# Kernel optimization log

Measured on AMD Instinct MI355X. Metric: run time of the kernel, lower is better.

Reference implementation:

```python
import jax, jax.numpy as jnp
import numpy as np

B, T, D, H = 8, 1024, 512, 8
HD = D // H  # per-head hidden = embed_dim // n_head = 64
EPS = 1e-5


def setup_inputs() -> dict:
    key = jax.random.key(0)
    ks = jax.random.split(key, 8)
    x = jax.random.normal(ks[0], (B, T, D), dtype=jnp.float32)
    sc = 1.0 / np.sqrt(D)
    Wq = jax.random.normal(ks[1], (D, H * HD), dtype=jnp.float32) * sc
    Wk = jax.random.normal(ks[2], (D, H * HD), dtype=jnp.float32) * sc
    Wp = jax.random.normal(ks[3], (H * HD, D), dtype=jnp.float32) * sc
    bq = jnp.zeros((H * HD,), jnp.float32)
    bk = jnp.zeros((H * HD,), jnp.float32)
    bp = jnp.zeros((D,), jnp.float32)
    w_mlp = jax.random.normal(ks[4], (2 * HD,), dtype=jnp.float32) * 0.1
    ln_g = jnp.ones((D,), jnp.float32)
    ln_b = jnp.zeros((D,), jnp.float32)
    return {"x": x, "Wq": Wq, "bq": bq, "Wk": Wk, "bk": bk,
            "Wp": Wp, "bp": bp, "w_mlp": w_mlp, "ln_g": ln_g, "ln_b": ln_b}


def reference(x, Wq, bq, Wk, bk, Wp, bp, w_mlp, ln_g, ln_b):
    b, t, d = x.shape
    h, hd = H, HD
    # q/k projections, split into heads: [B,T,H,hd]
    qx = (x @ Wq + bq).reshape(b, t, h, hd)
    kx = (x @ Wk + bk).reshape(b, t, h, hd)
    # MLP score: tanh(concat(k_j, q_i) . w) == tanh(k_j.w[:hd] + q_i.w[hd:])
    k_s = jnp.einsum('bkhd,d->bkh', kx, w_mlp[:hd])   # [B,K,H]
    q_s = jnp.einsum('bqhd,d->bqh', qx, w_mlp[hd:])   # [B,Q,H]
    score = jnp.tanh(q_s[:, :, None, :] + k_s[:, None, :, :])  # [B,Q,K,H]
    attn = jax.nn.softmax(score, axis=2)  # softmax over k_len
    # values are the key projection kx (bmm(score, kx) in original)
    out = jnp.einsum('bqkh,bkhd->bqhd', attn, kx).reshape(b, t, h * hd)
    out = out @ Wp + bp  # output projection (dropout is identity at eval)
    # residual + LayerNorm
    y = x + out
    mu = jnp.mean(y, axis=-1, keepdims=True)
    var = jnp.var(y, axis=-1, keepdims=True)
    yn = (y - mu) * jax.lax.rsqrt(var + EPS)
    return yn * ln_g + ln_b
```

## Files before the change

kernel.cpp:

```cpp
#include <hip/hip_runtime.h>
#include <cstddef>

#define TT 1024
#define DDIM 512
#define HH 8
#define NND 128
#define NS 68

typedef __attribute__((ext_vector_type(8))) short bfrag;
typedef __attribute__((ext_vector_type(4))) float facc;

#define SC2   2.8853900817779268f
#define L2E   1.4426950408889634f

static __device__ __forceinline__ unsigned bfrne(float f) {
    unsigned u = __float_as_uint(f);
    return (u + 0x7fffu + ((u >> 16) & 1u)) >> 16;
}
static __device__ __forceinline__ unsigned pack2rne(float a, float b) {
    return bfrne(a) | (bfrne(b) << 16);
}
static __device__ __forceinline__ unsigned pack2hu(float a, float b) {
    return ((__float_as_uint(a) + 0x8000u) >> 16) |
           ((__float_as_uint(b) + 0x8000u) & 0xffff0000u);
}
static __device__ __forceinline__ void gl2lds16(const void* g, void* l) {
    __builtin_amdgcn_global_load_lds(
        (const __attribute__((address_space(1))) unsigned int*)g,
        (__attribute__((address_space(3))) unsigned int*)l, 16, 0, 0);
}
static __device__ __forceinline__ float wfun(float z2) {
    float t = __builtin_amdgcn_exp2f(z2);
    float r = __builtin_amdgcn_rcpf(t + 1.f);
    return __builtin_amdgcn_exp2f(fmaf(r, -2.f * L2E, L2E));
}

__global__ __launch_bounds__(256) void prepare_kernel(
    const float* __restrict__ x, const float* __restrict__ Wk,
    const float* __restrict__ Wp, const float* __restrict__ Wq,
    const float* __restrict__ bq, const float* __restrict__ wm,
    unsigned short* __restrict__ xb, unsigned short* __restrict__ WkT,
    unsigned short* __restrict__ WpT, unsigned short* __restrict__ vq2b,
    float* __restrict__ qsb2)
{
    const int bx = blockIdx.x, tid = threadIdx.x;
    if (bx < 2048) {
        const int lane = tid & 63, wave = tid >> 6;
        const int row = bx * 4 + wave;
        const float4* xr = (const float4*)(x + (size_t)row * DDIM);
        float4 x0 = xr[lane * 2], x1 = xr[lane * 2 + 1];
        uint4 st;
        st.x = pack2rne(x0.x, x0.y); st.y = pack2rne(x0.z, x0.w);
        st.z = pack2rne(x1.x, x1.y); st.w = pack2rne(x1.z, x1.w);
        int p = lane ^ (row & 7);
        *(uint4*)(xb + (size_t)row * DDIM + p * 8) = st;
    } else if (bx < 2176) {
        int idx = bx - 2048;
        const float* src = (idx & 64) ? Wp : Wk;
        unsigned short* dst = (idx & 64) ? WpT : WkT;
        idx &= 63;
        const int n0 = (idx & 7) * 64, k0 = (idx >> 3) * 64;
        __shared__ float sT[64][65];
        #pragma unroll
        for (int it = 0; it < 4; ++it) {
            int task = it * 256 + tid;
            int kr = task >> 4, c4 = (task & 15) * 4;
            float4 v = *(const float4*)(src + (size_t)(k0 + kr) * DDIM + n0 + c4);
            sT[kr][c4] = v.x; sT[kr][c4 + 1] = v.y; sT[kr][c4 + 2] = v.z; sT[kr][c4 + 3] = v.w;
        }
        __syncthreads();
        #pragma unroll
        for (int it = 0; it < 2; ++it) {
            int task = it * 256 + tid;
            int n = task >> 3, kg = task & 7;
            unsigned u[4];
            #pragma unroll
            for (int jj = 0; jj < 4; ++jj)
                u[jj] = pack2rne(sT[kg * 8 + jj * 2][n], sT[kg * 8 + jj * 2 + 1][n]);
            int p = ((k0 >> 3) + kg) ^ (n & 7);
            uint4 st; st.x = u[0]; st.y = u[1]; st.z = u[2]; st.w = u[3];
            *(uint4*)(dst + (size_t)(n0 + n) * DDIM + p * 8) = st;
        }
    } else {
        int idx = (bx - 2176) * 256 + tid;
        int h = idx >> 9, d = idx & 511;
        float s = 0.f;
        #pragma unroll 8
        for (int j = 0; j < 64; ++j)
            s = fmaf(Wq[(size_t)d * DDIM + h * 64 + j], wm[64 + j], s);
        vq2b[h * DDIM + d] = (unsigned short)bfrne(s * SC2);
        if (idx < HH) {
            float sb = 0.f;
            for (int j = 0; j < 64; ++j)
                sb = fmaf(bq[idx * 64 + j], wm[64 + j], sb);
            qsb2[idx] = sb * SC2;
        }
    }
}

__global__ __launch_bounds__(256) void gemm1_kernel(
    const unsigned short* __restrict__ A, const unsigned short* __restrict__ B,
    const float* __restrict__ bias, unsigned short* __restrict__ kxTg,
    float* __restrict__ ks2, const float* __restrict__ wm,
    const unsigned short* __restrict__ vq2b, const float* __restrict__ qsb2,
    float* __restrict__ qs2)
{
    __shared__ __align__(16) unsigned short smem[17408];
    unsigned short* sA = smem;
    unsigned short* sB = smem + 8192;
    const int tid = threadIdx.x, lane = tid & 63, wave = tid >> 6;
    const int l15 = lane & 15, quad = lane >> 4;
    const int wr = wave >> 1, wc = wave & 1;
    const int row0 = blockIdx.x * 128, colpair = blockIdx.y;
    const int h = colpair * 2 + wc, n0 = colpair * 128;

    facc acc[4][4]; facc accq[4];
    #pragma unroll
    for (int i = 0; i < 4; ++i) {
        #pragma unroll
        for (int j = 0; j < 4; ++j) { acc[i][j][0]=0.f; acc[i][j][1]=0.f; acc[i][j][2]=0.f; acc[i][j][3]=0.f; }
        accq[i][0]=0.f; accq[i][1]=0.f; accq[i][2]=0.f; accq[i][3]=0.f;
    }

    for (int k0 = 0; k0 < 512; k0 += 64) {
        #pragma unroll
        for (int it = 0; it < 4; ++it) {
            int g = it * 256 + tid;
            int r = g >> 3, kg = g & 7;
            gl2lds16(A + (size_t)(row0 + r) * 512 + k0 + kg * 8, &sA[g * 8]);
            gl2lds16(B + (size_t)(n0 + r) * 512 + k0 + kg * 8, &sB[g * 8]);
        }
        __syncthreads();
        #pragma unroll
        for (int ks_ = 0; ks_ < 2; ++ks_) {
            int slot = (ks_ * 4 + quad) ^ (l15 & 7);
            bfrag a[4], b[4];
            #pragma unroll
            for (int i = 0; i < 4; ++i) {
                a[i] = *(const bfrag*)&sA[(wr * 64 + i * 16 + l15) * 64 + slot * 8];
                b[i] = *(const bfrag*)&sB[(wc * 64 + i * 16 + l15) * 64 + slot * 8];
            }
            bfrag bvq = *(const bfrag*)(vq2b + h * 512 + k0 + ks_ * 32 + quad * 8);
            #pragma unroll
            for (int i = 0; i < 4; ++i) {
                #pragma unroll
                for (int nt = 0; nt < 4; ++nt)
                    acc[i][nt] = __builtin_amdgcn_mfma_f32_16x16x32_bf16(a[i], b[nt], acc[i][nt], 0, 0, 0);
                accq[i] = __builtin_amdgcn_mfma_f32_16x16x32_bf16(a[i], bvq, accq[i], 0, 0, 0);
            }
        }
        __syncthreads();
    }

    const int bb = row0 >> 10, t0 = row0 & 1023;
    const float qsbh = qsb2[h];
    float bvv[4], wmv[4];
    #pragma unroll
    for (int nt = 0; nt < 4; ++nt) {
        bvv[nt] = bias[h * 64 + nt * 16 + l15];
        wmv[nt] = wm[nt * 16 + l15] * SC2;
    }
    float part[4][4];
    #pragma unroll
    for (int i = 0; i < 4; ++i)
        #pragma unroll
        for (int r = 0; r < 4; ++r) part[i][r] = 0.f;

    unsigned short* eT = smem + wc * 8704;
    #pragma unroll
    for (int i = 0; i < 4; ++i) {
        int tr = wr * 64 + i * 16 + quad * 4;
        #pragma unroll
        for (int nt = 0; nt < 4; ++nt) {
            int d = nt * 16 + l15;
            float v0 = acc[i][nt][0] + bvv[nt], v1 = acc[i][nt][1] + bvv[nt];
            float v2 = acc[i][nt][2] + bvv[nt], v3 = acc[i][nt][3] + bvv[nt];
            part[i][0] = fmaf(wmv[nt], v0, part[i][0]);
            part[i][1] = fmaf(wmv[nt], v1, part[i][1]);
            part[i][2] = fmaf(wmv[nt], v2, part[i][2]);
            part[i][3] = fmaf(wmv[nt], v3, part[i][3]);
            *(unsigned*)&eT[d * 136 + tr]     = pack2rne(v0, v1);
            *(unsigned*)&eT[d * 136 + tr + 2] = pack2rne(v2, v3);
        }
    }
    #pragma unroll
    for (int i = 0; i < 4; ++i)
        #pragma unroll
        for (int r = 0; r < 4; ++r) {
            float p = part[i][r];
            p += __shfl_xor(p, 1); p += __shfl_xor(p, 2);
            p += __shfl_xor(p, 4); p += __shfl_xor(p, 8);
            if (l15 == 0) {
                size_t o = (size_t)(bb * HH + h) * TT + t0 + wr * 64 + i * 16 + quad * 4 + r;
                ks2[o] = p;
                qs2[o] = accq[i][r] + qsbh;
            }
        }
    __syncthreads();
    #pragma unroll
    for (int it = 0; it < 8; ++it) {
        int task = it * 256 + tid;
        int hh = task >> 10, rem = task & 1023;
        int col = rem >> 4, seg = rem & 15;
        uint4 v = *(const uint4*)&smem[hh * 8704 + col * 136 + seg * 8];
        int hg = colpair * 2 + hh;
        int g = (t0 >> 3) + seg;
        int p = g ^ (col & 7);
        *(uint4*)(kxTg + ((size_t)(bb * HH + hg) * 64 + col) * TT + p * 8) = v;
    }
}

__global__ __launch_bounds__(256) void attn_kernel(
    const unsigned short* __restrict__ kxTg, const float* __restrict__ qs2,
    const float* __restrict__ ks2, unsigned short* __restrict__ attb)
{
    __shared__ __align__(16) unsigned short kxT[64 * 256];
    __shared__ float ksc[1024];
    __shared__ float redl[8];
    __shared__ __align__(16) float nodes[NND * NS];
    const int bh = blockIdx.x, thalf = blockIdx.y;
    const int b = bh >> 3, h = bh & 7;
    const int tid = threadIdx.x, lane = tid & 63, wave = tid >> 6;
    const int l15 = lane & 15, quad = lane >> 4;

    ((float4*)ksc)[tid] = ((const float4*)(ks2 + (size_t)bh * TT))[tid];
    float4 q4 = ((const float4*)(qs2 + (size_t)bh * TT))[tid];
    float mn = fminf(fminf(q4.x, q4.y), fminf(q4.z, q4.w));
    float mx = fmaxf(fmaxf(q4.x, q4.y), fmaxf(q4.z, q4.w));
    #pragma unroll
    for (int off = 32; off > 0; off >>= 1) {
        mn = fminf(mn, __shfl_xor(mn, off));
        mx = fmaxf(mx, __shfl_xor(mx, off));
    }
    if (lane == 0) { redl[wave] = mn; redl[4 + wave] = mx; }
    __syncthreads();
    const float mnv = fminf(fminf(redl[0], redl[1]), fminf(redl[2], redl[3]));
    const float mxv = fmaxf(fmaxf(redl[4], redl[5]), fmaxf(redl[6], redl[7]));
    const float h2v = (mxv - mnv) * (1.f / 127.f);
    const float inv127v = 127.f / fmaxf(mxv - mnv, 1e-12f);
    const float zA = mnv + (wave * 16 + l15) * h2v;
    const float zB = zA + 64.f * h2v;

    const unsigned short* kxbase = kxTg + (size_t)bh * 64 * TT;
    facc acc[2][4]; facc accZ[2];
    #pragma unroll
    for (int g = 0; g < 2; ++g) {
        #pragma unroll
        for (int i = 0; i < 4; ++i) { acc[g][i][0]=0.f; acc[g][i][1]=0.f; acc[g][i][2]=0.f; acc[g][i][3]=0.f; }
        accZ[g][0]=0.f; accZ[g][1]=0.f; accZ[g][2]=0.f; accZ[g][3]=0.f;
    }
    bfrag ones;
    #pragma unroll
    for (int j = 0; j < 8; ++j) ones[j] = (short)0x3F80;

    for (int ck = 0; ck < 4; ++ck) {
        #pragma unroll
        for (int it = 0; it < 8; ++it) {
            int g = it * 256 + tid;
            int d = g >> 5, j = g & 31;
            gl2lds16(kxbase + (size_t)d * TT + ck * 256 + j * 8, &kxT[g * 8]);
        }
        __syncthreads();
        #pragma unroll
        for (int kst = 0; kst < 8; ++kst) {
            const float* kvp = &ksc[ck * 256 + kst * 32 + quad * 8];
            float4 kv0 = *(const float4*)kvp;
            float4 kv1 = *(const float4*)(kvp + 4);
            int slot = (kst * 4 + quad) ^ (l15 & 7);
            bfrag bf_[4];
            #pragma unroll
            for (int dt = 0; dt < 4; ++dt)
                bf_[dt] = *(const bfrag*)&kxT[(dt * 16 + l15) * 256 + slot * 8];
            #pragma unroll
            for (int g = 0; g < 2; ++g) {
                float z = g ? zB : zA;
                union { unsigned u[4]; bfrag f; } afu;
                afu.u[0] = pack2hu(wfun(z + kv0.x), wfun(z + kv0.y));
                afu.u[1] = pack2hu(wfun(z + kv0.z), wfun(z + kv0.w));
                afu.u[2] = pack2hu(wfun(z + kv1.x), wfun(z + kv1.y));
                afu.u[3] = pack2hu(wfun(z + kv1.z), wfun(z + kv1.w));
                #pragma unroll
                for (int dt = 0; dt < 4; ++dt)
                    acc[g][dt] = __builtin_amdgcn_mfma_f32_16x16x32_bf16(afu.f, bf_[dt], acc[g][dt], 0, 0, 0);
                accZ[g] = __builtin_amdgcn_mfma_f32_16x16x32_bf16(afu.f, ones, accZ[g], 0, 0, 0);
            }
        }
        __syncthreads();
    }
    #pragma unroll
    for (int g = 0; g < 2; ++g) {
        #pragma unroll
        for (int r = 0; r < 4; ++r) {
            int node = g * 64 + wave * 16 + quad * 4 + r;
            #pragma unroll
            for (int dt = 0; dt < 4; ++dt)
                nodes[node * NS + dt * 16 + l15] = acc[g][dt][r];
            if (l15 == 0) nodes[node * NS + 64] = accZ[g][r];
        }
    }
    __syncthreads();

    const float* qsp = qs2 + (size_t)bh * TT;
    #pragma unroll 2
    for (int it = 0; it < 32; ++it) {
        int task = it * 256 + tid;
        int t = thalf * 512 + (task >> 4), dp = task & 15;
        float qv = qsp[t];
        float u = (qv - mnv) * inv127v;
        int i = (int)floorf(u) - 1;
        i = i < 0 ? 0 : (i > NND - 4 ? NND - 4 : i);
        float s = u - (float)i;
        float s1 = s - 1.f, s2 = s - 2.f, s3 = s - 3.f;
        float w0 = -s1 * s2 * s3 * (1.f / 6.f);
        float w1 = s * s2 * s3 * 0.5f;
        float w2 = -s * s1 * s3 * 0.5f;
        float w3 = s * s1 * s2 * (1.f / 6.f);
        const float* base = &nodes[i * NS];
        float4 v0 = *(const float4*)(base + 4 * dp);
        float4 v1 = *(const float4*)(base + NS + 4 * dp);
        float4 v2 = *(const float4*)(base + 2 * NS + 4 * dp);
        float4 v3 = *(const float4*)(base + 3 * NS + 4 * dp);
        float zz = w0 * base[64] + w1 * base[NS + 64] + w2 * base[2 * NS + 64] + w3 * base[3 * NS + 64];
        float ox = w0 * v0.x + w1 * v1.x + w2 * v2.x + w3 * v3.x;
        float oy = w0 * v0.y + w1 * v1.y + w2 * v2.y + w3 * v3.y;
        float oz = w0 * v0.z + w1 * v1.z + w2 * v2.z + w3 * v3.z;
        float ow = w0 * v0.w + w1 * v1.w + w2 * v2.w + w3 * v3.w;
        float rz = __builtin_amdgcn_rcpf(zz);
        uint2 st;
        st.x = pack2rne(ox * rz, oy * rz);
        st.y = pack2rne(oz * rz, ow * rz);
        int row = b * TT + t;
        int col = h * 64 + 4 * dp;
        int p = (col >> 3) ^ (row & 7);
        *(uint2*)&attb[(size_t)row * DDIM + p * 8 + (col & 7)] = st;
    }
}

__global__ __launch_bounds__(256) void gemm2_kernel(
    const unsigned short* __restrict__ A, const unsigned short* __restrict__ B,
    const float* __restrict__ bias, unsigned short* __restrict__ yb)
{
    __shared__ __align__(16) unsigned short smem[17408];
    unsigned short* sA = smem;
    unsigned short* sB = smem + 8192;
    const int tid = threadIdx.x, lane = tid & 63, wave = tid >> 6;
    const int l15 = lane & 15, quad = lane >> 4;
    const int wr = wave >> 1, wc = wave & 1;
    const int row0 = blockIdx.x * 128, col0 = blockIdx.y * 128;

    facc acc[4][4];
    #pragma unroll
    for (int i = 0; i < 4; ++i)
        #pragma unroll
        for (int j = 0; j < 4; ++j) { acc[i][j][0]=0.f; acc[i][j][1]=0.f; acc[i][j][2]=0.f; acc[i][j][3]=0.f; }

    for (int k0 = 0; k0 < 512; k0 += 64) {
        #pragma unroll
        for (int it = 0; it < 4; ++it) {
            int g = it * 256 + tid;
            int r = g >> 3, kg = g & 7;
            gl2lds16(A + (size_t)(row0 + r) * 512 + k0 + kg * 8, &sA[g * 8]);
            gl2lds16(B + (size_t)(col0 + r) * 512 + k0 + kg * 8, &sB[g * 8]);
        }
        __syncthreads();
        #pragma unroll
        for (int ks_ = 0; ks_ < 2; ++ks_) {
            int slot = (ks_ * 4 + quad) ^ (l15 & 7);
            bfrag a[4], b[4];
            #pragma unroll
            for (int i = 0; i < 4; ++i) {
                a[i] = *(const bfrag*)&sA[(wr * 64 + i * 16 + l15) * 64 + slot * 8];
                b[i] = *(const bfrag*)&sB[(wc * 64 + i * 16 + l15) * 64 + slot * 8];
            }
            #pragma unroll
            for (int i = 0; i < 4; ++i)
                #pragma unroll
                for (int nt = 0; nt < 4; ++nt)
                    acc[i][nt] = __builtin_amdgcn_mfma_f32_16x16x32_bf16(a[i], b[nt], acc[i][nt], 0, 0, 0);
        }
        __syncthreads();
    }
    float bvv[4];
    #pragma unroll
    for (int nt = 0; nt < 4; ++nt) bvv[nt] = bias[col0 + wc * 64 + nt * 16 + l15];
    unsigned short* yT = smem;
    #pragma unroll
    for (int i = 0; i < 4; ++i) {
        #pragma unroll
        for (int nt = 0; nt < 4; ++nt) {
            int col = wc * 64 + nt * 16 + l15;
            #pragma unroll
            for (int r = 0; r < 4; ++r) {
                int row = wr * 64 + i * 16 + quad * 4 + r;
                yT[row * 136 + col] = (unsigned short)bfrne(acc[i][nt][r] + bvv[nt]);
            }
        }
    }
    __syncthreads();
    #pragma unroll
    for (int it = 0; it < 8; ++it) {
        int task = it * 256 + tid;
        int row = task >> 4, seg = task & 15;
        uint4 v = *(const uint4*)&yT[row * 136 + seg * 8];
        *(uint4*)(yb + (size_t)(row0 + row) * DDIM + col0 + seg * 8) = v;
    }
}

__global__ __launch_bounds__(256) void ln_kernel(
    const unsigned short* __restrict__ yb, const unsigned short* __restrict__ xb,
    const float* __restrict__ g, const float* __restrict__ bet,
    float* __restrict__ out)
{
    const int tid = threadIdx.x, lane = tid & 63, wave = tid >> 6;
    const int row = blockIdx.x * 4 + wave;
    uint4 pv = *(const uint4*)(yb + (size_t)row * DDIM + lane * 8);
    int pgr = lane ^ (row & 7);
    uint4 xv = *(const uint4*)(xb + (size_t)row * DDIM + pgr * 8);
    float y[8];
    const unsigned* pu = (const unsigned*)&pv;
    const unsigned* xu = (const unsigned*)&xv;
    #pragma unroll
    for (int j = 0; j < 4; ++j) {
        y[2*j]   = __uint_as_float(pu[j] << 16)        + __uint_as_float(xu[j] << 16);
        y[2*j+1] = __uint_as_float(pu[j] & 0xffff0000u) + __uint_as_float(xu[j] & 0xffff0000u);
    }
    float s = 0.f, s2 = 0.f;
    #pragma unroll
    for (int i = 0; i < 8; ++i) { s += y[i]; s2 = fmaf(y[i], y[i], s2); }
    #pragma unroll
    for (int off = 32; off > 0; off >>= 1) {
        s += __shfl_xor(s, off);
        s2 += __shfl_xor(s2, off);
    }
    float mu = s * (1.f / 512.f);
    float var = s2 * (1.f / 512.f) - mu * mu;
    float inv = rsqrtf(var + 1e-5f);
    const float4* gp = (const float4*)(g + lane * 8);
    const float4* bp = (const float4*)(bet + lane * 8);
    float4 g0 = gp[0], g1 = gp[1], b0 = bp[0], b1 = bp[1];
    float4 o0, o1;
    o0.x = (y[0] - mu) * inv * g0.x + b0.x; o0.y = (y[1] - mu) * inv * g0.y + b0.y;
    o0.z = (y[2] - mu) * inv * g0.z + b0.z; o0.w = (y[3] - mu) * inv * g0.w + b0.w;
    o1.x = (y[4] - mu) * inv * g1.x + b1.x; o1.y = (y[5] - mu) * inv * g1.y + b1.y;
    o1.z = (y[6] - mu) * inv * g1.z + b1.z; o1.w = (y[7] - mu) * inv * g1.w + b1.w;
    float4* op = (float4*)(out + (size_t)row * DDIM);
    op[lane * 2] = o0; op[lane * 2 + 1] = o1;
}

extern "C" void kernel_launch(void* const* d_in, const int* in_sizes, int n_in,
                              void* d_out, int out_size, void* d_ws, size_t ws_size,
                              hipStream_t stream)
{
    const float* x    = (const float*)d_in[0];
    const float* Wq   = (const float*)d_in[1];
    const float* bq   = (const float*)d_in[2];
    const float* Wk   = (const float*)d_in[3];
    const float* bk   = (const float*)d_in[4];
    const float* Wp   = (const float*)d_in[5];
    const float* bp   = (const float*)d_in[6];
    const float* wm   = (const float*)d_in[7];
    const float* ln_g = (const float*)d_in[8];
    const float* ln_b = (const float*)d_in[9];
    float* out = (float*)d_out;

    float* ws = (float*)d_ws;
    float*          qsb2 = ws;
    unsigned short* vq2b = (unsigned short*)(ws + 64);
    unsigned short* WkT  = (unsigned short*)(ws + 2112);
    unsigned short* WpT  = (unsigned short*)(ws + 133184);
    unsigned short* xb   = (unsigned short*)(ws + 264256);
    unsigned short* kxTg = (unsigned short*)(ws + 2361408);
    float*          qs2  = ws + 4458560;
    float*          ks2  = ws + 4524096;
    unsigned short* attb = (unsigned short*)(ws + 4589632);
    unsigned short* yb   = (unsigned short*)(ws + 6686784);

    prepare_kernel<<<2192, 256, 0, stream>>>(x, Wk, Wp, Wq, bq, wm,
                                             xb, WkT, WpT, vq2b, qsb2);
    gemm1_kernel<<<dim3(64, 4), 256, 0, stream>>>(xb, WkT, bk, kxTg, ks2, wm,
                                                  vq2b, qsb2, qs2);
    attn_kernel<<<dim3(64, 2), 256, 0, stream>>>(kxTg, qs2, ks2, attb);
    gemm2_kernel<<<dim3(64, 4), 256, 0, stream>>>(attb, WpT, bp, yb);
    ln_kernel<<<2048, 256, 0, stream>>>(yb, xb, ln_g, ln_b, out);
}
```

Measured before the change: 153.7 us.

## Double-buffer LDS tiles in both GEMMs and attention with async prefetch

Gives gemm1, gemm2 and attn_kernel double-buffered shared-memory tiles, so the next K-chunk is loaded with global-to-LDS copies while the current one is consumed. The old sync-load-sync loop becomes a manual vmcnt wait plus raw barriers. gemm1 also stages the vq2b vector in LDS instead of reading it from global memory on every step, and bias/wm loads are hoisted ahead of the main loop. The cost is roughly double the LDS per block, which may reduce occupancy, and more fragile hand-written waitcnt synchronisation.

```diff
diff --git a/kernel.cpp b/kernel.cpp
--- a/kernel.cpp
+++ b/kernel.cpp
@@ -105,15 +105,22 @@
     const unsigned short* __restrict__ vq2b, const float* __restrict__ qsb2,
     float* __restrict__ qs2)
 {
-    __shared__ __align__(16) unsigned short smem[17408];
-    unsigned short* sA = smem;
-    unsigned short* sB = smem + 8192;
+    __shared__ __align__(16) unsigned short smem[33792];
+    unsigned short* svq = smem + 32768;
     const int tid = threadIdx.x, lane = tid & 63, wave = tid >> 6;
     const int l15 = lane & 15, quad = lane >> 4;
     const int wr = wave >> 1, wc = wave & 1;
     const int row0 = blockIdx.x * 128, colpair = blockIdx.y;
     const int h = colpair * 2 + wc, n0 = colpair * 128;
 
+    const float qsbh = qsb2[h];
+    float bvv[4], wmv[4];
+    #pragma unroll
+    for (int nt = 0; nt < 4; ++nt) {
+        bvv[nt] = bias[h * 64 + nt * 16 + l15];
+        wmv[nt] = wm[nt * 16 + l15] * SC2;
+    }
+
     facc acc[4][4]; facc accq[4];
     #pragma unroll
     for (int i = 0; i < 4; ++i) {
@@ -122,15 +129,34 @@
         accq[i][0]=0.f; accq[i][1]=0.f; accq[i][2]=0.f; accq[i][3]=0.f;
     }
 
-    for (int k0 = 0; k0 < 512; k0 += 64) {
+    if (tid < 128)
+        gl2lds16(vq2b + colpair * 1024 + tid * 8, &svq[tid * 8]);
+
+    auto stage = [&](int sel, int k0) {
+        unsigned short* dA = smem + sel * 16384;
+        unsigned short* dB = dA + 8192;
         #pragma unroll
         for (int it = 0; it < 4; ++it) {
             int g = it * 256 + tid;
             int r = g >> 3, kg = g & 7;
-            gl2lds16(A + (size_t)(row0 + r) * 512 + k0 + kg * 8, &sA[g * 8]);
-            gl2lds16(B + (size_t)(n0 + r) * 512 + k0 + kg * 8, &sB[g * 8]);
-        }
-        __syncthreads();
+            gl2lds16(A + (size_t)(row0 + r) * 512 + k0 + kg * 8, &dA[g * 8]);
+            gl2lds16(B + (size_t)(n0 + r) * 512 + k0 + kg * 8, &dB[g * 8]);
+        }
+    };
+
+    stage(0, 0);
+    for (int kt = 0; kt < 8; ++kt) {
+        const int sel = kt & 1;
+        if (kt < 7) {
+            stage(sel ^ 1, (kt + 1) * 64);
+            asm volatile("s_waitcnt vmcnt(8)" ::: "memory");
+        } else {
+            asm volatile("s_waitcnt vmcnt(0)" ::: "memory");
+        }
+        __builtin_amdgcn_s_barrier();
+        __builtin_amdgcn_sched_barrier(0);
+        const unsigned short* sA = smem + sel * 16384;
+        const unsigned short* sB = sA + 8192;
         #pragma unroll
         for (int ks_ = 0; ks_ < 2; ++ks_) {
             int slot = (ks_ * 4 + quad) ^ (l15 & 7);
@@ -140,7 +166,7 @@
                 a[i] = *(const bfrag*)&sA[(wr * 64 + i * 16 + l15) * 64 + slot * 8];
                 b[i] = *(const bfrag*)&sB[(wc * 64 + i * 16 + l15) * 64 + slot * 8];
             }
-            bfrag bvq = *(const bfrag*)(vq2b + h * 512 + k0 + ks_ * 32 + quad * 8);
+            bfrag bvq = *(const bfrag*)&svq[wc * 512 + kt * 64 + ks_ * 32 + quad * 8];
             #pragma unroll
             for (int i = 0; i < 4; ++i) {
                 #pragma unroll
@@ -149,17 +175,12 @@
                 accq[i] = __builtin_amdgcn_mfma_f32_16x16x32_bf16(a[i], bvq, accq[i], 0, 0, 0);
             }
         }
-        __syncthreads();
-    }
+        __builtin_amdgcn_s_barrier();
+        __builtin_amdgcn_sched_barrier(0);
+    }
+    asm volatile("" ::: "memory");
 
     const int bb = row0 >> 10, t0 = row0 & 1023;
-    const float qsbh = qsb2[h];
-    float bvv[4], wmv[4];
-    #pragma unroll
-    for (int nt = 0; nt < 4; ++nt) {
-        bvv[nt] = bias[h * 64 + nt * 16 + l15];
-        wmv[nt] = wm[nt * 16 + l15] * SC2;
-    }
     float part[4][4];
     #pragma unroll
     for (int i = 0; i < 4; ++i)
@@ -214,7 +235,7 @@
     const unsigned short* __restrict__ kxTg, const float* __restrict__ qs2,
     const float* __restrict__ ks2, unsigned short* __restrict__ attb)
 {
-    __shared__ __align__(16) unsigned short kxT[64 * 256];
+    __shared__ __align__(16) unsigned short kxT[2 * 64 * 256];
     __shared__ float ksc[1024];
     __shared__ float redl[8];
     __shared__ __align__(16) float nodes[NND * NS];
@@ -222,9 +243,22 @@
     const int b = bh >> 3, h = bh & 7;
     const int tid = threadIdx.x, lane = tid & 63, wave = tid >> 6;
     const int l15 = lane & 15, quad = lane >> 4;
-
-    ((float4*)ksc)[tid] = ((const float4*)(ks2 + (size_t)bh * TT))[tid];
-    float4 q4 = ((const float4*)(qs2 + (size_t)bh * TT))[tid];
+    const unsigned short* kxbase = kxTg + (size_t)bh * 64 * TT;
+
+    auto stage = [&](int sel, int ck) {
+        unsigned short* dst = kxT + sel * 16384;
+        #pragma unroll
+        for (int it = 0; it < 8; ++it) {
+            int g = it * 256 + tid;
+            int d = g >> 5, j = g & 31;
+            gl2lds16(kxbase + (size_t)d * TT + ck * 256 + j * 8, &dst[g * 8]);
+        }
+    };
+
+    float4 ks4 = ((const float4*)(ks2 + (size_t)bh * TT))[tid];
+    float4 q4  = ((const float4*)(qs2 + (size_t)bh * TT))[tid];
+    stage(0, 0);
+    ((float4*)ksc)[tid] = ks4;
     float mn = fminf(fminf(q4.x, q4.y), fminf(q4.z, q4.w));
     float mx = fmaxf(fmaxf(q4.x, q4.y), fmaxf(q4.z, q4.w));
     #pragma unroll
@@ -233,7 +267,9 @@
         mx = fmaxf(mx, __shfl_xor(mx, off));
     }
     if (lane == 0) { redl[wave] = mn; redl[4 + wave] = mx; }
-    __syncthreads();
+    asm volatile("s_waitcnt lgkmcnt(0)" ::: "memory");
+    __builtin_amdgcn_s_barrier();
+    __builtin_amdgcn_sched_barrier(0);
     const float mnv = fminf(fminf(redl[0], redl[1]), fminf(redl[2], redl[3]));
     const float mxv = fmaxf(fmaxf(redl[4], redl[5]), fmaxf(redl[6], redl[7]));
     const float h2v = (mxv - mnv) * (1.f / 127.f);
@@ -241,7 +277,6 @@
     const float zA = mnv + (wave * 16 + l15) * h2v;
     const float zB = zA + 64.f * h2v;
 
-    const unsigned short* kxbase = kxTg + (size_t)bh * 64 * TT;
     facc acc[2][4]; facc accZ[2];
     #pragma unroll
     for (int g = 0; g < 2; ++g) {
@@ -254,13 +289,16 @@
     for (int j = 0; j < 8; ++j) ones[j] = (short)0x3F80;
 
     for (int ck = 0; ck < 4; ++ck) {
-        #pragma unroll
-        for (int it = 0; it < 8; ++it) {
-            int g = it * 256 + tid;
-            int d = g >> 5, j = g & 31;
-            gl2lds16(kxbase + (size_t)d * TT + ck * 256 + j * 8, &kxT[g * 8]);
-        }
-        __syncthreads();
+        const int sel = ck & 1;
+        if (ck < 3) {
+            stage(sel ^ 1, ck + 1);
+            asm volatile("s_waitcnt vmcnt(8)" ::: "memory");
+        } else {
+            asm volatile("s_waitcnt vmcnt(0)" ::: "memory");
+        }
+        __builtin_amdgcn_s_barrier();
+        __builtin_amdgcn_sched_barrier(0);
+        const unsigned short* kx = kxT + sel * 16384;
         #pragma unroll
         for (int kst = 0; kst < 8; ++kst) {
             const float* kvp = &ksc[ck * 256 + kst * 32 + quad * 8];
@@ -270,7 +308,7 @@
             bfrag bf_[4];
             #pragma unroll
             for (int dt = 0; dt < 4; ++dt)
-                bf_[dt] = *(const bfrag*)&kxT[(dt * 16 + l15) * 256 + slot * 8];
+                bf_[dt] = *(const bfrag*)&kx[(dt * 16 + l15) * 256 + slot * 8];
             #pragma unroll
             for (int g = 0; g < 2; ++g) {
                 float z = g ? zB : zA;
@@ -285,8 +323,10 @@
                 accZ[g] = __builtin_amdgcn_mfma_f32_16x16x32_bf16(afu.f, ones, accZ[g], 0, 0, 0);
             }
         }
-        __syncthreads();
-    }
+        __builtin_amdgcn_s_barrier();
+        __builtin_amdgcn_sched_barrier(0);
+    }
+    asm volatile("" ::: "memory");
     #pragma unroll
     for (int g = 0; g < 2; ++g) {
         #pragma unroll
@@ -340,29 +380,47 @@
     const unsigned short* __restrict__ A, const unsigned short* __restrict__ B,
     const float* __restrict__ bias, unsigned short* __restrict__ yb)
 {
-    __shared__ __align__(16) unsigned short smem[17408];
-    unsigned short* sA = smem;
-    unsigned short* sB = smem + 8192;
+    __shared__ __align__(16) unsigned short smem[32768];
     const int tid = threadIdx.x, lane = tid & 63, wave = tid >> 6;
     const int l15 = lane & 15, quad = lane >> 4;
     const int wr = wave >> 1, wc = wave & 1;
     const int row0 = blockIdx.x * 128, col0 = blockIdx.y * 128;
 
+    float bvv[4];
+    #pragma unroll
+    for (int nt = 0; nt < 4; ++nt) bvv[nt] = bias[col0 + wc * 64 + nt * 16 + l15];
+
     facc acc[4][4];
     #pragma unroll
     for (int i = 0; i < 4; ++i)
         #pragma unroll
         for (int j = 0; j < 4; ++j) { acc[i][j][0]=0.f; acc[i][j][1]=0.f; acc[i][j][2]=0.f; acc[i][j][3]=0.f; }
 
-    for (int k0 = 0; k0 < 512; k0 += 64) {
+    auto stage = [&](int sel, int k0) {
+        unsigned short* dA = smem + sel * 16384;
+        unsigned short* dB = dA + 8192;
         #pragma unroll
         for (int it = 0; it < 4; ++it) {
             int g = it * 256 + tid;
             int r = g >> 3, kg = g & 7;
-            gl2lds16(A + (size_t)(row0 + r) * 512 + k0 + kg * 8, &sA[g * 8]);
-            gl2lds16(B + (size_t)(col0 + r) * 512 + k0 + kg * 8, &sB[g * 8]);
-        }
-        __syncthreads();
+            gl2lds16(A + (size_t)(row0 + r) * 512 + k0 + kg * 8, &dA[g * 8]);
+            gl2lds16(B + (size_t)(col0 + r) * 512 + k0 + kg * 8, &dB[g * 8]);
+        }
+    };
+
+    stage(0, 0);
+    for (int kt = 0; kt < 8; ++kt) {
+        const int sel = kt & 1;
+        if (kt < 7) {
+            stage(sel ^ 1, (kt + 1) * 64);
+            asm volatile("s_waitcnt vmcnt(8)" ::: "memory");
+        } else {
+            asm volatile("s_waitcnt vmcnt(0)" ::: "memory");
+        }
+        __builtin_amdgcn_s_barrier();
+        __builtin_amdgcn_sched_barrier(0);
+        const unsigned short* sA = smem + sel * 16384;
+        const unsigned short* sB = sA + 8192;
         #pragma unroll
         for (int ks_ = 0; ks_ < 2; ++ks_) {
             int slot = (ks_ * 4 + quad) ^ (l15 & 7);
@@ -378,11 +436,11 @@
                 for (int nt = 0; nt < 4; ++nt)
                     acc[i][nt] = __builtin_amdgcn_mfma_f32_16x16x32_bf16(a[i], b[nt], acc[i][nt], 0, 0, 0);
         }
-        __syncthreads();
-    }
-    float bvv[4];
-    #pragma unroll
-    for (int nt = 0; nt < 4; ++nt) bvv[nt] = bias[col0 + wc * 64 + nt * 16 + l15];
+        __builtin_amdgcn_s_barrier();
+        __builtin_amdgcn_sched_barrier(0);
+    }
+    asm volatile("" ::: "memory");
+
     unsigned short* yT = smem;
     #pragma unroll
     for (int i = 0; i < 4; ++i) {
```

After: 139.9 us. -9.0%, faster.
